# Performance work log

Measured on AMD Instinct MI355X. Metric: run time of the kernel, lower is better.

Reference implementation:

```python
import jax, jax.numpy as jnp
import numpy as np

B, T, D, H = 64, 1024, 256, 256
FLF, STEP_RED = 0.5, 0.2


def _segment(x_np):
    """Iterative variance-based segmenter (host-side numpy, mirrors the
    detached torch code: data-dependent shapes, non-differentiable)."""
    B_, T_, D_ = x_np.shape
    enc = np.concatenate([np.zeros((1, D_), np.float32), x_np.reshape(-1, D_)], 0)
    cs1 = np.cumsum(enc, 0)
    cs2 = np.cumsum(enc * enc, 0)
    idx = np.arange(cs1.shape[0], dtype=np.int64)
    final_length = int(FLF * enc.shape[0])
    while idx.shape[0] > final_length:
        begs, ends = idx[:-2], idx[2:]
        s1 = cs1[ends] - cs1[begs]
        s2 = cs2[ends] - cs2[begs]
        n = (ends - begs).astype(np.float32)[:, None]
        var = (s2 / n - (s1 / n) ** 2).mean(1)
        diffs = np.sqrt(np.maximum(var, 0.0))  # clamp tiny fp32 negatives
        diffs = np.concatenate([[1e10], diffs, [1e10]]).astype(np.float32)
        k = max(final_length, int(idx.shape[0] * STEP_RED))
        keep = np.sort(np.argsort(-diffs, kind='stable')[:k])
        idx = idx[keep]
    seq_end = np.arange(0, B_ * T_, T_, dtype=np.int64)
    idx = np.unique(np.concatenate([idx, seq_end]))
    cut = np.nonzero(idx % T_ == 0)[0]          # B_+1 cutpoints (0 and each seq start/end)
    lens = np.diff(cut)                          # segments per batch element
    rel = idx[1:] % T_
    groups = np.split(rel, np.cumsum(lens)[:-1])
    Lc = int(lens.max())
    seq = np.zeros((B_, Lc), np.int64)
    for b, g in enumerate(groups):
        seq[b, :len(g)] = g
    seq[seq == 0] = T_                           # seq end / padding -> T
    seq = np.concatenate([np.zeros((B_, 1), np.int64), seq], 1)
    fr = np.arange(T_)[None, None, :]
    # cm[b, j, t] = 1 iff frame t belongs to segment j of sequence b
    cm = ((seq[:, :-1, None] <= fr) & (seq[:, 1:, None] > fr)).astype(np.float32)
    return cm


def _gru(x, W_ih, W_hh, b_ih, b_hh):
    # x: [B, L, D]; torch GRU gate packing order: (r, z, n)
    h0 = jnp.zeros((x.shape[0], W_hh.shape[1]), x.dtype)

    def step(h, xt):
        gi = xt @ W_ih.T + b_ih
        gh = h @ W_hh.T + b_hh
        i_r, i_z, i_n = jnp.split(gi, 3, -1)
        h_r, h_z, h_n = jnp.split(gh, 3, -1)
        r = jax.nn.sigmoid(i_r + h_r)
        z = jax.nn.sigmoid(i_z + h_z)
        n = jnp.tanh(i_n + r * h_n)
        h_new = (1.0 - z) * n + z * h
        return h_new, h_new

    _, out = jax.lax.scan(step, h0, jnp.swapaxes(x, 0, 1))  # [L, B, H]
    return jnp.swapaxes(out, 0, 1)


def setup_inputs() -> dict:
    key = jax.random.key(0)
    k = jax.random.split(key, 5)
    s = 1.0 / np.sqrt(H)  # torch.nn.GRU default uniform init bound
    return {
        'x': jax.random.normal(k[0], (B, T, D), jnp.float32),
        'W_ih': jax.random.uniform(k[1], (3 * H, D), jnp.float32, -s, s),
        'W_hh': jax.random.uniform(k[2], (3 * H, H), jnp.float32, -s, s),
        'b_ih': jax.random.uniform(k[3], (3 * H,), jnp.float32, -s, s),
        'b_hh': jax.random.uniform(k[4], (3 * H,), jnp.float32, -s, s),
    }


def reference(x, W_ih, W_hh, b_ih, b_hh):
    # 1) segment (detached, data-dependent -> host numpy, like torch's python loop)
    cm = jnp.asarray(_segment(np.asarray(x)))  # [B, Lc, T]
    # 2) compress: mean of frames within each segment
    norm = cm / jnp.maximum(cm.sum(-1, keepdims=True), 1.0)
    comp = jnp.einsum('blt,btd->bld', norm, x)
    # 3) GRU over compressed sequence (padded segments feed zeros; their
    #    outputs receive zero weight in decompress, matching packed-seq math)
    out = _gru(comp, W_ih, W_hh, b_ih, b_hh)  # [B, Lc, H]
    # 4) decompress: broadcast each segment's output back to its frames
    return jnp.einsum('blt,blh->bth', cm, out)  # [B, T, H]
```

## Files before the change

kernel.cpp:

```cpp
#include <hip/hip_runtime.h>
#include <cstdint>
#include <cstddef>
#include <cmath>


#define NPOS 65537
#define KSEL 32768u

typedef _Float16 f16x2 __attribute__((ext_vector_type(2)));
typedef _Float16 f16x8 __attribute__((ext_vector_type(8)));

#if defined(__has_builtin)
#if __has_builtin(__builtin_amdgcn_fdot2)
#define HAVE_FDOT2 1
#endif
#endif

__device__ __forceinline__ float fdot2f(f16x2 a, f16x2 b, float c) {
#ifdef HAVE_FDOT2
  return __builtin_amdgcn_fdot2(a, b, c, false);
#else
  c += (float)a.x * (float)b.x;
  c += (float)a.y * (float)b.y;
  return c;
#endif
}

__global__ __launch_bounds__(256) void k_warm(const float4* __restrict__ x4,
                                              float* __restrict__ sink) {
  size_t i = (size_t)blockIdx.x * 256 + threadIdx.x;
  float4 v = x4[i];
  float s = (v.x + v.y) + (v.z + v.w);
  if (s == 1.23456789e-33f) sink[0] = s;
}

__global__ __launch_bounds__(256) void k_carry(const float* __restrict__ x,
                                               float* __restrict__ carr) {
  __shared__ __align__(16) float lds[2 * 256 * 64];
  const int b = blockIdx.x;
  const int sq = b >> 2;
  const int j0 = (b & 3) * 64;
  const int wid = threadIdx.x >> 6;
  const int l = threadIdx.x & 63;

  if (wid != 0) {
    const int wsel = wid - 1;
    const size_t lane_off = (size_t)(l >> 4) * 256 + (size_t)(l & 15) * 4;
    for (int c = 0; c <= 256; ++c) {
      if (c < 256) {
        const float* src = x + (size_t)c * 256 * 256 + j0 + lane_off;
        float* dbase = lds + (c & 1) * 16384;
        for (int g = wsel; g < 64; g += 3) {
          __builtin_amdgcn_global_load_lds(
              (const __attribute__((address_space(1))) void*)(src + (size_t)g * 1024),
              (__attribute__((address_space(3))) void*)(dbase + g * 256),
              16, 0, 0);
        }
      }
      asm volatile("s_waitcnt vmcnt(0)" ::: "memory");
      __builtin_amdgcn_sched_barrier(0);
      __builtin_amdgcn_s_barrier();
      __builtin_amdgcn_sched_barrier(0);
    }
  } else {
#pragma clang fp contract(off)
    __builtin_amdgcn_s_barrier();
    __builtin_amdgcn_sched_barrier(0);
    float acc = 0.f;
    float* cw = carr + ((size_t)sq * 256) * 256 + j0 + l;
    if (sq) {
      for (int c = 0; c < 256; ++c) {
        cw[(size_t)c * 256] = acc;
        const float* lp = lds + (c & 1) * 16384 + l;
#pragma unroll 16
        for (int r = 0; r < 256; ++r) {
          float v = lp[r * 64];
          v = v * v;
          acc = acc + v;
        }
        asm volatile("s_waitcnt lgkmcnt(0)" ::: "memory");
        __builtin_amdgcn_sched_barrier(0);
        __builtin_amdgcn_s_barrier();
        __builtin_amdgcn_sched_barrier(0);
      }
    } else {
      for (int c = 0; c < 256; ++c) {
        cw[(size_t)c * 256] = acc;
        const float* lp = lds + (c & 1) * 16384 + l;
#pragma unroll 16
        for (int r = 0; r < 256; ++r) {
          float v = lp[r * 64];
          acc = acc + v;
        }
        asm volatile("s_waitcnt lgkmcnt(0)" ::: "memory");
        __builtin_amdgcn_sched_barrier(0);
        __builtin_amdgcn_s_barrier();
        __builtin_amdgcn_sched_barrier(0);
      }
    }
  }
}

__global__ __launch_bounds__(256) void k_spread(const float* __restrict__ x,
                                                const float* __restrict__ carr,
                                                float* __restrict__ cs1,
                                                float* __restrict__ cs2) {
#pragma clang fp contract(off)
  const int blk = blockIdx.x;
  const int sq = blk >> 8;
  const int ch = blk & 255;
  const int col = threadIdx.x;
  float* dst = sq ? cs2 : cs1;
  float c = carr[((size_t)sq * 256 + ch) * 256 + col];
  const float* gp = x + (size_t)ch * 256 * 256 + col;
  float* sp = dst + ((size_t)ch * 256 + 1) * 256 + col;
  if (ch == 0) dst[col] = 0.f;
  float buf[4][8];
#pragma unroll
  for (int d = 0; d < 3; ++d)
#pragma unroll
    for (int u = 0; u < 8; ++u)
      buf[d][u] = gp[(size_t)(d * 8 + u) * 256];
  for (int g = 0; g < 8; ++g) {
#pragma unroll
    for (int d = 0; d < 4; ++d) {
      const int s = g * 4 + d;
      if (s + 3 < 32) {
        const float* ld = gp + (size_t)(s + 3) * 8 * 256;
#pragma unroll
        for (int u = 0; u < 8; ++u)
          buf[(d + 3) & 3][u] = ld[(size_t)u * 256];
      }
#pragma unroll
      for (int u = 0; u < 8; ++u) {
        float v = buf[d][u];
        if (sq) v = v * v;
        c = c + v;
        sp[(size_t)(s * 8 + u) * 256] = c;
      }
    }
  }
}

__device__ __forceinline__ float dterm(float ap, float am, float bp, float bm) {
#pragma clang fp contract(off)
  float s1 = ap - am;
  float s2 = bp - bm;
  float t1 = s1 * 0.5f;
  float u = s2 * 0.5f;
  return u - t1 * t1;
}

__global__ __launch_bounds__(64) void k_diffs(const float* __restrict__ cs1,
                                              const float* __restrict__ cs2,
                                              float* __restrict__ diffs) {
#pragma clang fp contract(off)
  int p = blockIdx.x * 64 + threadIdx.x;
  if (p >= NPOS) return;
  if (p == 0 || p == NPOS - 1) { diffs[p] = 1e10f; return; }
  const float4* am4 = (const float4*)(cs1 + (size_t)(p - 1) * 256);
  const float4* ap4 = (const float4*)(cs1 + (size_t)(p + 1) * 256);
  const float4* bm4 = (const float4*)(cs2 + (size_t)(p - 1) * 256);
  const float4* bp4 = (const float4*)(cs2 + (size_t)(p + 1) * 256);
  float blk[2];
  for (int half = 0; half < 2; ++half) {
    float r[8];
    for (int i = 0; i < 16; ++i) {
      int q = half * 32 + i * 2;
      float4 a0 = ap4[q], m0 = am4[q], b0 = bp4[q], n0 = bm4[q];
      float4 a1 = ap4[q + 1], m1 = am4[q + 1], b1 = bp4[q + 1], n1 = bm4[q + 1];
      float e0 = dterm(a0.x, m0.x, b0.x, n0.x);
      float e1 = dterm(a0.y, m0.y, b0.y, n0.y);
      float e2 = dterm(a0.z, m0.z, b0.z, n0.z);
      float e3 = dterm(a0.w, m0.w, b0.w, n0.w);
      float e4 = dterm(a1.x, m1.x, b1.x, n1.x);
      float e5 = dterm(a1.y, m1.y, b1.y, n1.y);
      float e6 = dterm(a1.z, m1.z, b1.z, n1.z);
      float e7 = dterm(a1.w, m1.w, b1.w, n1.w);
      if (i == 0) {
        r[0] = e0; r[1] = e1; r[2] = e2; r[3] = e3;
        r[4] = e4; r[5] = e5; r[6] = e6; r[7] = e7;
      } else {
        r[0] += e0; r[1] += e1; r[2] += e2; r[3] += e3;
        r[4] += e4; r[5] += e5; r[6] += e6; r[7] += e7;
      }
    }
    blk[half] = ((r[0] + r[1]) + (r[2] + r[3])) + ((r[4] + r[5]) + (r[6] + r[7]));
  }
  float mean = (blk[0] + blk[1]) / 256.0f;
  float mx = mean > 0.0f ? mean : 0.0f;
  diffs[p] = (float)::sqrt((double)mx);
}

__global__ void k_hist1(const float* __restrict__ diffs, unsigned* __restrict__ h1) {
  int p = blockIdx.x * 256 + threadIdx.x;
  if (p >= NPOS) return;
  unsigned key = __float_as_uint(diffs[p]);
  atomicAdd(&h1[key >> 16], 1u);
}

__global__ void k_sel_hi(const unsigned* __restrict__ h1, unsigned* __restrict__ meta) {
  __shared__ unsigned loc[256];
  int t = threadIdx.x;
  unsigned s = 0;
  for (int i = 0; i < 256; ++i) s += h1[t * 256 + i];
  loc[t] = s;
  __syncthreads();
  if (t == 0) {
    unsigned run = 0; int tt = 255;
    for (; tt > 0; --tt) { if (run + loc[tt] >= KSEL) break; run += loc[tt]; }
    unsigned r2 = run;
    for (int i = 255; i >= 0; --i) {
      unsigned c = h1[tt * 256 + i];
      if (r2 + c >= KSEL) { meta[0] = (unsigned)(tt * 256 + i); meta[1] = r2; break; }
      r2 += c;
    }
  }
}

__global__ void k_hist2(const float* __restrict__ diffs, const unsigned* __restrict__ meta,
                        unsigned* __restrict__ h2) {
  int p = blockIdx.x * 256 + threadIdx.x;
  if (p >= NPOS) return;
  unsigned key = __float_as_uint(diffs[p]);
  if ((key >> 16) == meta[0]) atomicAdd(&h2[key & 0xffffu], 1u);
}

__global__ void k_sel_lo(const unsigned* __restrict__ h2, unsigned* __restrict__ meta) {
  __shared__ unsigned loc[256];
  int t = threadIdx.x;
  unsigned s = 0;
  for (int i = 0; i < 256; ++i) s += h2[t * 256 + i];
  loc[t] = s;
  __syncthreads();
  if (t == 0) {
    unsigned remaining = KSEL - meta[1];
    unsigned run = 0; int tt = 255;
    for (; tt > 0; --tt) { if (run + loc[tt] >= remaining) break; run += loc[tt]; }
    unsigned r2 = run;
    for (int i = 255; i >= 0; --i) {
      unsigned c = h2[tt * 256 + i];
      if (r2 + c >= remaining) {
        meta[2] = (meta[0] << 16) | (unsigned)(tt * 256 + i);
        meta[3] = remaining - r2;
        break;
      }
      r2 += c;
    }
  }
}

__global__ __launch_bounds__(64) void k_keep(const float* __restrict__ diffs,
                                             const unsigned* __restrict__ meta,
                                             unsigned char* __restrict__ keep) {
  int lane = threadIdx.x;
  unsigned Kstar = meta[2], need = meta[3];
  unsigned base = 0;
  float v[4], nv[4];
#pragma unroll
  for (int q = 0; q < 4; ++q) nv[q] = diffs[q * 64 + lane];
  for (int it = 0; it < 257; ++it) {
#pragma unroll
    for (int q = 0; q < 4; ++q) v[q] = nv[q];
    if (it < 256) {
      int nb = (it + 1) * 256;
#pragma unroll
      for (int q = 0; q < 4; ++q) {
        int idx = nb + q * 64 + lane;
        nv[q] = (idx < NPOS) ? diffs[idx] : 0.f;
      }
    }
#pragma unroll
    for (int q = 0; q < 4; ++q) {
      int p = it * 256 + q * 64 + lane;
      bool valid = p < NPOS;
      unsigned key = valid ? __float_as_uint(v[q]) : 0u;
      bool eq = valid && (key == Kstar);
      unsigned long long m = __ballot(eq);
      unsigned rank = base + (unsigned)__popcll(m & ((1ull << lane) - 1ull));
      bool k = valid && ((key > Kstar) || (eq && rank < need) || ((p & 1023) == 0));
      if (valid) keep[p] = (unsigned char)k;
      base += (unsigned)__popcll(m);
    }
  }
}

__global__ __launch_bounds__(1024) void k_segment(const unsigned char* __restrict__ keep,
                                                  int* __restrict__ segid,
                                                  int* __restrict__ bnd,
                                                  int* __restrict__ nseg) {
  __shared__ int s[1024];
  int b = blockIdx.x, t = threadIdx.x;
  int f = (t >= 1) ? (int)keep[b * 1024 + t] : 0;
  s[t] = f;
  __syncthreads();
  for (int off = 1; off < 1024; off <<= 1) {
    int v = s[t];
    int add = (t >= off) ? s[t - off] : 0;
    __syncthreads();
    s[t] = v + add;
    __syncthreads();
  }
  int sc = s[t];
  segid[b * 1024 + t] = sc;
  if (f) bnd[b * 1026 + sc] = t;
  if (t == 0) bnd[b * 1026] = 0;
  if (t == 1023) {
    int m = sc + 1;
    nseg[b] = m;
    bnd[b * 1026 + m] = 1024;
  }
}

__global__ __launch_bounds__(64) void k_prefix(const int* __restrict__ nseg,
                                               int* __restrict__ pref) {
  int lane = threadIdx.x;
  int s = nseg[lane];
  for (int off = 1; off < 64; off <<= 1) {
    int u = __shfl_up(s, off);
    if (lane >= off) s += u;
  }
  pref[lane + 1] = s;
  if (lane == 0) pref[0] = 0;
}

__global__ __launch_bounds__(256) void k_pool(const float* __restrict__ x,
                                              const int* __restrict__ bnd,
                                              const int* __restrict__ nseg,
                                              const int* __restrict__ pref,
                                              float* __restrict__ comp) {
  int d = threadIdx.x;
  for (int s = 0; s < 32; ++s) {
    int sid = blockIdx.x * 32 + s;
    int b = sid >> 10, li = sid & 1023;
    if (li >= nseg[b]) continue;
    int s0 = bnd[b * 1026 + li], e0 = bnd[b * 1026 + li + 1];
    float acc = 0.f;
    for (int t = s0; t < e0; ++t) acc += x[((size_t)b * 1024 + t) * 256 + d];
    comp[((size_t)pref[b] + li) * 256 + d] = acc / (float)(e0 - s0);
  }
}

__global__ __launch_bounds__(256) void k_gi(const float* __restrict__ comp,
                                            const float* __restrict__ Wih,
                                            const float* __restrict__ bih,
                                            const float* __restrict__ bhh,
                                            const int* __restrict__ pref,
                                            float* __restrict__ gi) {
  int total = pref[64];
  int r0 = blockIdx.x * 64;
  if (r0 >= total) return;
  int c0 = blockIdx.y * 128;
  __shared__ float As[64][64];
  __shared__ float Bs[64 * 132];
  int tid = threadIdx.x;
  int rg = tid >> 5, cl = tid & 31;
  float acc[8][4];
#pragma unroll
  for (int i = 0; i < 8; ++i)
#pragma unroll
    for (int q = 0; q < 4; ++q) acc[i][q] = 0.f;

  for (int k0 = 0; k0 < 256; k0 += 64) {
#pragma unroll
    for (int i = 0; i < 4; ++i) {
      int idx = tid + i * 256;
      int row = idx >> 4, kq = idx & 15;
      int rr = r0 + row;
      float4 v;
      if (rr < total) v = *reinterpret_cast<const float4*>(comp + (size_t)rr * 256 + k0 + kq * 4);
      else { v.x = 0.f; v.y = 0.f; v.z = 0.f; v.w = 0.f; }
      *reinterpret_cast<float4*>(&As[row][kq * 4]) = v;
    }
#pragma unroll
    for (int i = 0; i < 8; ++i) {
      int idx = tid + i * 256;
      int row = idx >> 4, kq = idx & 15;
      float4 v = *reinterpret_cast<const float4*>(Wih + (size_t)(c0 + row) * 256 + k0 + kq * 4);
      Bs[(kq * 4 + 0) * 132 + row] = v.x;
      Bs[(kq * 4 + 1) * 132 + row] = v.y;
      Bs[(kq * 4 + 2) * 132 + row] = v.z;
      Bs[(kq * 4 + 3) * 132 + row] = v.w;
    }
    __syncthreads();
#pragma unroll 4
    for (int k = 0; k < 64; ++k) {
      float a[8], bv[4];
#pragma unroll
      for (int i = 0; i < 8; ++i) a[i] = As[rg * 8 + i][k];
#pragma unroll
      for (int q = 0; q < 4; ++q) bv[q] = Bs[k * 132 + cl + 32 * q];
#pragma unroll
      for (int i = 0; i < 8; ++i)
#pragma unroll
        for (int q = 0; q < 4; ++q) acc[i][q] += a[i] * bv[q];
    }
    __syncthreads();
  }
#pragma unroll
  for (int q = 0; q < 4; ++q) {
    int c = c0 + cl + 32 * q;
    float bias = bih[c] + (c < 512 ? bhh[c] : 0.f);
#pragma unroll
    for (int i = 0; i < 8; ++i) {
      int rr = r0 + rg * 8 + i;
      if (rr < total) gi[(size_t)rr * 768 + c] = acc[i][q] + bias;
    }
  }
}

__global__ __attribute__((amdgpu_waves_per_eu(2, 2)))
__launch_bounds__(512) void k_gru(const float* __restrict__ gi,
                                  const float* __restrict__ Whh,
                                  const float* __restrict__ bhh,
                                  const int* __restrict__ nseg,
                                  const int* __restrict__ pref,
                                  float* __restrict__ gout) {
  const int b = blockIdx.x;
  const int t = threadIdx.x;
  const int m = nseg[b];
  const size_t base = (size_t)pref[b];
  const int half = t >> 8;
  const int pr = t & 255;
  const int k0 = half * 128;

  f16x2 wr[64], wz[64], wn[64];
#pragma unroll
  for (int i = 0; i < 32; ++i) {
    float4 v = *(const float4*)(Whh + (size_t)pr * 256 + k0 + i * 4);
    f16x2 ra; ra.x = (_Float16)v.x; ra.y = (_Float16)v.y; wr[2 * i] = ra;
    f16x2 rb; rb.x = (_Float16)v.z; rb.y = (_Float16)v.w; wr[2 * i + 1] = rb;
    float4 u = *(const float4*)(Whh + (size_t)(256 + pr) * 256 + k0 + i * 4);
    f16x2 za; za.x = (_Float16)u.x; za.y = (_Float16)u.y; wz[2 * i] = za;
    f16x2 zb; zb.x = (_Float16)u.z; zb.y = (_Float16)u.w; wz[2 * i + 1] = zb;
    float4 q = *(const float4*)(Whh + (size_t)(512 + pr) * 256 + k0 + i * 4);
    f16x2 na; na.x = (_Float16)q.x; na.y = (_Float16)q.y; wn[2 * i] = na;
    f16x2 nb; nb.x = (_Float16)q.z; nb.y = (_Float16)q.w; wn[2 * i + 1] = nb;
  }

  __shared__ f16x8 hbuf8[32];
  __shared__ float2 pp2[768];

  float bn = (t < 256) ? bhh[512 + t] : 0.f;
  float hreg = 0.f;
  if (t < 32) {
    f16x8 z = (f16x8)(_Float16)0.f;
    hbuf8[t] = z;
  }
  __syncthreads();

  float cr = 0.f, cz = 0.f, cn = 0.f;
  if (t < 256) {
    const float* g0 = gi + base * 768;
    cr = g0[t]; cz = g0[256 + t]; cn = g0[512 + t];
  }

  for (int l = 0; l < m; ++l) {
    float nr = 0.f, nz = 0.f, nn = 0.f;
    if (t < 256 && l + 1 < m) {
      const float* g1 = gi + (base + l + 1) * 768;
      nr = g1[t]; nz = g1[256 + t]; nn = g1[512 + t];
    }
    float ar0 = 0.f, ar1 = 0.f, az0 = 0.f, az1 = 0.f, an0 = 0.f, an1 = 0.f;
#pragma unroll
    for (int i = 0; i < 16; ++i) {
      f16x8 hv = hbuf8[half * 16 + i];
      f16x2 p0; p0.x = hv[0]; p0.y = hv[1];
      f16x2 p1; p1.x = hv[2]; p1.y = hv[3];
      f16x2 p2; p2.x = hv[4]; p2.y = hv[5];
      f16x2 p3; p3.x = hv[6]; p3.y = hv[7];
      ar0 = fdot2f(wr[4 * i + 0], p0, ar0);
      ar1 = fdot2f(wr[4 * i + 1], p1, ar1);
      ar0 = fdot2f(wr[4 * i + 2], p2, ar0);
      ar1 = fdot2f(wr[4 * i + 3], p3, ar1);
      az0 = fdot2f(wz[4 * i + 0], p0, az0);
      az1 = fdot2f(wz[4 * i + 1], p1, az1);
      az0 = fdot2f(wz[4 * i + 2], p2, az0);
      az1 = fdot2f(wz[4 * i + 3], p3, az1);
      an0 = fdot2f(wn[4 * i + 0], p0, an0);
      an1 = fdot2f(wn[4 * i + 1], p1, an1);
      an0 = fdot2f(wn[4 * i + 2], p2, an0);
      an1 = fdot2f(wn[4 * i + 3], p3, an1);
    }
    float* ppf = (float*)pp2;
    ppf[pr * 2 + half] = ar0 + ar1;
    ppf[(256 + pr) * 2 + half] = az0 + az1;
    ppf[(512 + pr) * 2 + half] = an0 + an1;
    asm volatile("s_waitcnt lgkmcnt(0)" ::: "memory");
    __builtin_amdgcn_sched_barrier(0);
    __builtin_amdgcn_s_barrier();
    __builtin_amdgcn_sched_barrier(0);
    if (t < 256) {
      float2 qr = pp2[t];
      float2 qz = pp2[256 + t];
      float2 qn = pp2[512 + t];
      float sr = qr.x + qr.y;
      float sz = qz.x + qz.y;
      float sn = qn.x + qn.y + bn;
      float r = 1.f / (1.f + __expf(-(cr + sr)));
      float z = 1.f / (1.f + __expf(-(cz + sz)));
      float arg = cn + r * sn;
      float n = 2.f / (1.f + __expf(-2.f * arg)) - 1.f;
      float hnew = (1.f - z) * n + z * hreg;
      hreg = hnew;
      ((_Float16*)hbuf8)[t] = (_Float16)hnew;
      gout[(base + l) * 256 + t] = hnew;
    }
    cr = nr; cz = nz; cn = nn;
    asm volatile("s_waitcnt lgkmcnt(0)" ::: "memory");
    __builtin_amdgcn_sched_barrier(0);
    __builtin_amdgcn_s_barrier();
    __builtin_amdgcn_sched_barrier(0);
  }
}

__global__ __launch_bounds__(256) void k_scatter(const float* __restrict__ gout,
                                                 const int* __restrict__ segid,
                                                 const int* __restrict__ pref,
                                                 float* __restrict__ out) {
  int d = threadIdx.x;
  for (int rr = 0; rr < 32; ++rr) {
    int row = blockIdx.x * 32 + rr;
    int b = row >> 10;
    int l = segid[row];
    out[(size_t)row * 256 + d] = gout[((size_t)pref[b] + l) * 256 + d];
  }
}

extern "C" void kernel_launch(void* const* d_in, const int* in_sizes, int n_in,
                              void* d_out, int out_size, void* d_ws, size_t ws_size,
                              hipStream_t stream) {
  const float* x   = (const float*)d_in[0];
  const float* Wih = (const float*)d_in[1];
  const float* Whh = (const float*)d_in[2];
  const float* bih = (const float*)d_in[3];
  const float* bhh = (const float*)d_in[4];
  float* out = (float*)d_out;
  char* w = (char*)d_ws;

  const size_t o_cs1   = 0;
  const size_t o_cs2   = 67110912;
  const size_t o_diffs = 134221824;
  const size_t o_h1    = 134484224;
  const size_t o_h2    = 134746368;
  const size_t o_meta  = 135008512;
  const size_t o_keep  = 135008768;
  const size_t o_segid = 135074560;
  const size_t o_bnd   = 135336704;
  const size_t o_nseg  = 135599360;
  const size_t o_pref  = 135599616;
  const size_t o_gi    = 135600128;
  const size_t NEED    = 236460032;
  if (ws_size < NEED) return;

  float* cs1 = (float*)(w + o_cs1);
  float* cs2 = (float*)(w + o_cs2);
  float* diffs = (float*)(w + o_diffs);
  unsigned* h1 = (unsigned*)(w + o_h1);
  unsigned* h2 = (unsigned*)(w + o_h2);
  unsigned* meta = (unsigned*)(w + o_meta);
  unsigned char* keep = (unsigned char*)(w + o_keep);
  int* segid = (int*)(w + o_segid);
  int* bnd = (int*)(w + o_bnd);
  int* nseg = (int*)(w + o_nseg);
  int* pref = (int*)(w + o_pref);
  float* gi = (float*)(w + o_gi);
  float* carr = (float*)(w + o_gi);
  float* comp = cs1;
  float* gout = cs2;
  float* sink = (float*)(w + o_meta + 192);

  hipMemsetAsync(h1, 0, 262144, stream);
  hipMemsetAsync(h2, 0, 262144, stream);

  k_warm   <<<dim3(16384),  dim3(256),  0, stream>>>((const float4*)x, sink);
  k_carry  <<<dim3(8),      dim3(256),  0, stream>>>(x, carr);
  k_spread <<<dim3(512),    dim3(256),  0, stream>>>(x, carr, cs1, cs2);
  k_diffs  <<<dim3(1025),   dim3(64),   0, stream>>>(cs1, cs2, diffs);
  k_hist1  <<<dim3(257),    dim3(256),  0, stream>>>(diffs, h1);
  k_sel_hi <<<dim3(1),      dim3(256),  0, stream>>>(h1, meta);
  k_hist2  <<<dim3(257),    dim3(256),  0, stream>>>(diffs, meta, h2);
  k_sel_lo <<<dim3(1),      dim3(256),  0, stream>>>(h2, meta);
  k_keep   <<<dim3(1),      dim3(64),   0, stream>>>(diffs, meta, keep);
  k_segment<<<dim3(64),     dim3(1024), 0, stream>>>(keep, segid, bnd, nseg);
  k_prefix <<<dim3(1),      dim3(64),   0, stream>>>(nseg, pref);
  k_pool   <<<dim3(2048),   dim3(256),  0, stream>>>(x, bnd, nseg, pref, comp);
  k_gi     <<<dim3(513, 6), dim3(256),  0, stream>>>(comp, Wih, bih, bhh, pref, gi);
  k_gru    <<<dim3(64),     dim3(512),  0, stream>>>(gi, Whh, bhh, nseg, pref, gout);
  k_scatter<<<dim3(2048),   dim3(256),  0, stream>>>(gout, segid, pref, out);
}
```

Before: 1.906 ms.

## Compute input-gate GEMM with fp16 MFMA instead of fp32 SIMT tiles

Stores the pooled segment means as fp16 and adds a kernel that converts W_ih to fp16. The input-projection GEMM is then rewritten to use 16x16x32 f16 MFMA instructions, loading fragments directly from global memory with no shared-memory staging. The aim is to cut the cost of the fp32 FMA-based GEMM that feeds the GRU. In exchange it loses input precision by rounding to fp16. It also writes rows past the valid total without a bounds check, since padding rows in the last tile are stored unguarded.

```diff
diff --git a/kernel.cpp b/kernel.cpp
--- a/kernel.cpp
+++ b/kernel.cpp
@@ -9,6 +9,8 @@
 
 typedef _Float16 f16x2 __attribute__((ext_vector_type(2)));
 typedef _Float16 f16x8 __attribute__((ext_vector_type(8)));
+typedef _Float16 frag8 __attribute__((ext_vector_type(8)));
+typedef float f32x4 __attribute__((ext_vector_type(4)));
 
 #if defined(__has_builtin)
 #if __has_builtin(__builtin_amdgcn_fdot2)
@@ -328,7 +330,7 @@
                                               const int* __restrict__ bnd,
                                               const int* __restrict__ nseg,
                                               const int* __restrict__ pref,
-                                              float* __restrict__ comp) {
+                                              _Float16* __restrict__ compH) {
   int d = threadIdx.x;
   for (int s = 0; s < 32; ++s) {
     int sid = blockIdx.x * 32 + s;
@@ -337,75 +339,64 @@
     int s0 = bnd[b * 1026 + li], e0 = bnd[b * 1026 + li + 1];
     float acc = 0.f;
     for (int t = s0; t < e0; ++t) acc += x[((size_t)b * 1024 + t) * 256 + d];
-    comp[((size_t)pref[b] + li) * 256 + d] = acc / (float)(e0 - s0);
-  }
-}
-
-__global__ __launch_bounds__(256) void k_gi(const float* __restrict__ comp,
-                                            const float* __restrict__ Wih,
-                                            const float* __restrict__ bih,
-                                            const float* __restrict__ bhh,
-                                            const int* __restrict__ pref,
-                                            float* __restrict__ gi) {
+    compH[((size_t)pref[b] + li) * 256 + d] = (_Float16)(acc / (float)(e0 - s0));
+  }
+}
+
+__global__ __launch_bounds__(256) void k_cvtw(const float* __restrict__ Wih,
+                                              _Float16* __restrict__ WihH) {
+  size_t i = (size_t)blockIdx.x * 256 + threadIdx.x;
+  WihH[i] = (_Float16)Wih[i];
+}
+
+__global__ __launch_bounds__(256) void k_gim(const _Float16* __restrict__ compH,
+                                             const _Float16* __restrict__ WihH,
+                                             const float* __restrict__ bih,
+                                             const float* __restrict__ bhh,
+                                             const int* __restrict__ pref,
+                                             float* __restrict__ gi) {
   int total = pref[64];
   int r0 = blockIdx.x * 64;
   if (r0 >= total) return;
-  int c0 = blockIdx.y * 128;
-  __shared__ float As[64][64];
-  __shared__ float Bs[64 * 132];
-  int tid = threadIdx.x;
-  int rg = tid >> 5, cl = tid & 31;
-  float acc[8][4];
-#pragma unroll
-  for (int i = 0; i < 8; ++i)
-#pragma unroll
-    for (int q = 0; q < 4; ++q) acc[i][q] = 0.f;
-
-  for (int k0 = 0; k0 < 256; k0 += 64) {
-#pragma unroll
-    for (int i = 0; i < 4; ++i) {
-      int idx = tid + i * 256;
-      int row = idx >> 4, kq = idx & 15;
-      int rr = r0 + row;
-      float4 v;
-      if (rr < total) v = *reinterpret_cast<const float4*>(comp + (size_t)rr * 256 + k0 + kq * 4);
-      else { v.x = 0.f; v.y = 0.f; v.z = 0.f; v.w = 0.f; }
-      *reinterpret_cast<float4*>(&As[row][kq * 4]) = v;
-    }
-#pragma unroll
-    for (int i = 0; i < 8; ++i) {
-      int idx = tid + i * 256;
-      int row = idx >> 4, kq = idx & 15;
-      float4 v = *reinterpret_cast<const float4*>(Wih + (size_t)(c0 + row) * 256 + k0 + kq * 4);
-      Bs[(kq * 4 + 0) * 132 + row] = v.x;
-      Bs[(kq * 4 + 1) * 132 + row] = v.y;
-      Bs[(kq * 4 + 2) * 132 + row] = v.z;
-      Bs[(kq * 4 + 3) * 132 + row] = v.w;
-    }
-    __syncthreads();
-#pragma unroll 4
-    for (int k = 0; k < 64; ++k) {
-      float a[8], bv[4];
-#pragma unroll
-      for (int i = 0; i < 8; ++i) a[i] = As[rg * 8 + i][k];
-#pragma unroll
-      for (int q = 0; q < 4; ++q) bv[q] = Bs[k * 132 + cl + 32 * q];
-#pragma unroll
-      for (int i = 0; i < 8; ++i)
-#pragma unroll
-        for (int q = 0; q < 4; ++q) acc[i][q] += a[i] * bv[q];
-    }
-    __syncthreads();
-  }
-#pragma unroll
-  for (int q = 0; q < 4; ++q) {
-    int c = c0 + cl + 32 * q;
-    float bias = bih[c] + (c < 512 ? bhh[c] : 0.f);
-#pragma unroll
-    for (int i = 0; i < 8; ++i) {
-      int rr = r0 + rg * 8 + i;
-      if (rr < total) gi[(size_t)rr * 768 + c] = acc[i][q] + bias;
-    }
+  int c0 = blockIdx.y * 64;
+  int wid = threadIdx.x >> 6;
+  int wr = wid >> 1, wc = wid & 1;
+  int l = threadIdx.x & 63;
+  int lrow = l & 15;
+  int koff = (l >> 4) * 8;
+
+  f32x4 acc00, acc01, acc10, acc11;
+#pragma unroll
+  for (int j = 0; j < 4; ++j) { acc00[j] = 0.f; acc01[j] = 0.f; acc10[j] = 0.f; acc11[j] = 0.f; }
+
+  const _Float16* aBase0 = compH + (size_t)(r0 + wr * 32 + lrow) * 256 + koff;
+  const _Float16* aBase1 = aBase0 + (size_t)16 * 256;
+  const _Float16* bBase0 = WihH + (size_t)(c0 + wc * 32 + lrow) * 256 + koff;
+  const _Float16* bBase1 = bBase0 + (size_t)16 * 256;
+
+#pragma unroll
+  for (int k0 = 0; k0 < 256; k0 += 32) {
+    frag8 a0 = *(const frag8*)(aBase0 + k0);
+    frag8 a1 = *(const frag8*)(aBase1 + k0);
+    frag8 b0 = *(const frag8*)(bBase0 + k0);
+    frag8 b1 = *(const frag8*)(bBase1 + k0);
+    acc00 = __builtin_amdgcn_mfma_f32_16x16x32_f16(a0, b0, acc00, 0, 0, 0);
+    acc01 = __builtin_amdgcn_mfma_f32_16x16x32_f16(a0, b1, acc01, 0, 0, 0);
+    acc10 = __builtin_amdgcn_mfma_f32_16x16x32_f16(a1, b0, acc10, 0, 0, 0);
+    acc11 = __builtin_amdgcn_mfma_f32_16x16x32_f16(a1, b1, acc11, 0, 0, 0);
+  }
+
+  int ccol0 = c0 + wc * 32 + (l & 15);
+  int crow0 = r0 + wr * 32 + (l >> 4) * 4;
+  float bias0 = bih[ccol0] + (ccol0 < 512 ? bhh[ccol0] : 0.f);
+  int ccol1 = ccol0 + 16;
+  float bias1 = bih[ccol1] + (ccol1 < 512 ? bhh[ccol1] : 0.f);
+#pragma unroll
+  for (int j = 0; j < 4; ++j) {
+    gi[(size_t)(crow0 + j) * 768 + ccol0] = acc00[j] + bias0;
+    gi[(size_t)(crow0 + j) * 768 + ccol1] = acc01[j] + bias1;
+    gi[(size_t)(crow0 + 16 + j) * 768 + ccol0] = acc10[j] + bias0;
+    gi[(size_t)(crow0 + 16 + j) * 768 + ccol1] = acc11[j] + bias1;
   }
 }
 
@@ -566,26 +557,28 @@
   int* pref = (int*)(w + o_pref);
   float* gi = (float*)(w + o_gi);
   float* carr = (float*)(w + o_gi);
-  float* comp = cs1;
+  _Float16* compH = (_Float16*)(w + o_cs1);
+  _Float16* WihH  = (_Float16*)(w + o_h1);
   float* gout = cs2;
   float* sink = (float*)(w + o_meta + 192);
 
   hipMemsetAsync(h1, 0, 262144, stream);
   hipMemsetAsync(h2, 0, 262144, stream);
 
-  k_warm   <<<dim3(16384),  dim3(256),  0, stream>>>((const float4*)x, sink);
-  k_carry  <<<dim3(8),      dim3(256),  0, stream>>>(x, carr);
-  k_spread <<<dim3(512),    dim3(256),  0, stream>>>(x, carr, cs1, cs2);
-  k_diffs  <<<dim3(1025),   dim3(64),   0, stream>>>(cs1, cs2, diffs);
-  k_hist1  <<<dim3(257),    dim3(256),  0, stream>>>(diffs, h1);
-  k_sel_hi <<<dim3(1),      dim3(256),  0, stream>>>(h1, meta);
-  k_hist2  <<<dim3(257),    dim3(256),  0, stream>>>(diffs, meta, h2);
-  k_sel_lo <<<dim3(1),      dim3(256),  0, stream>>>(h2, meta);
-  k_keep   <<<dim3(1),      dim3(64),   0, stream>>>(diffs, meta, keep);
-  k_segment<<<dim3(64),     dim3(1024), 0, stream>>>(keep, segid, bnd, nseg);
-  k_prefix <<<dim3(1),      dim3(64),   0, stream>>>(nseg, pref);
-  k_pool   <<<dim3(2048),   dim3(256),  0, stream>>>(x, bnd, nseg, pref, comp);
-  k_gi     <<<dim3(513, 6), dim3(256),  0, stream>>>(comp, Wih, bih, bhh, pref, gi);
-  k_gru    <<<dim3(64),     dim3(512),  0, stream>>>(gi, Whh, bhh, nseg, pref, gout);
-  k_scatter<<<dim3(2048),   dim3(256),  0, stream>>>(gout, segid, pref, out);
-}
+  k_warm   <<<dim3(16384),   dim3(256),  0, stream>>>((const float4*)x, sink);
+  k_carry  <<<dim3(8),       dim3(256),  0, stream>>>(x, carr);
+  k_spread <<<dim3(512),     dim3(256),  0, stream>>>(x, carr, cs1, cs2);
+  k_diffs  <<<dim3(1025),    dim3(64),   0, stream>>>(cs1, cs2, diffs);
+  k_hist1  <<<dim3(257),     dim3(256),  0, stream>>>(diffs, h1);
+  k_sel_hi <<<dim3(1),       dim3(256),  0, stream>>>(h1, meta);
+  k_hist2  <<<dim3(257),     dim3(256),  0, stream>>>(diffs, meta, h2);
+  k_sel_lo <<<dim3(1),       dim3(256),  0, stream>>>(h2, meta);
+  k_keep   <<<dim3(1),       dim3(64),   0, stream>>>(diffs, meta, keep);
+  k_segment<<<dim3(64),      dim3(1024), 0, stream>>>(keep, segid, bnd, nseg);
+  k_prefix <<<dim3(1),       dim3(64),   0, stream>>>(nseg, pref);
+  k_cvtw   <<<dim3(768),     dim3(256),  0, stream>>>(Wih, WihH);
+  k_pool   <<<dim3(2048),    dim3(256),  0, stream>>>(x, bnd, nseg, pref, compH);
+  k_gim    <<<dim3(513, 12), dim3(256),  0, stream>>>(compH, WihH, bih, bhh, pref, gi);
+  k_gru    <<<dim3(64),      dim3(512),  0, stream>>>(gi, Whh, bhh, nseg, pref, gout);
+  k_scatter<<<dim3(2048),    dim3(256),  0, stream>>>(gout, segid, pref, out);
+}
```

New measurement: 1.787 ms, median of 2. -6.3%, faster.
